# Kernel optimization log

Hardware: AMD Instinct MI355X
Metric: run time of the kernel (lower is better)

## Reference

```python
import jax, jax.numpy as jnp
import numpy as np

H = 1024      # hidden_dim
NH = 16       # num_heads
HD = H // NH  # head_dim
FFN = 4096
EPS = 1e-5


def setup_inputs() -> dict:
    key = jax.random.key(0)
    ks = jax.random.split(key, 12)
    s = 0.02
    return {
        "x": jax.random.normal(ks[0], (2, 2048, H), dtype=jnp.float32),
        "w_qkv": jax.random.normal(ks[1], (H, 3 * H), dtype=jnp.float32) * s,
        "b_qkv": jnp.zeros((3 * H,), dtype=jnp.float32),
        "w_out": jax.random.normal(ks[2], (H, H), dtype=jnp.float32) * s,
        "b_out": jnp.zeros((H,), dtype=jnp.float32),
        "ln1_g": jnp.ones((H,), dtype=jnp.float32),
        "ln1_b": jnp.zeros((H,), dtype=jnp.float32),
        "ln2_g": jnp.ones((H,), dtype=jnp.float32),
        "ln2_b": jnp.zeros((H,), dtype=jnp.float32),
        "w1": jax.random.normal(ks[3], (H, FFN), dtype=jnp.float32) * s,
        "b1": jnp.zeros((FFN,), dtype=jnp.float32),
        "w2": jax.random.normal(ks[4], (FFN, H), dtype=jnp.float32) * s,
        "b2": jnp.zeros((H,), dtype=jnp.float32),
    }


def _layernorm(x, g, b):
    mu = jnp.mean(x, axis=-1, keepdims=True)
    var = jnp.mean(jnp.square(x - mu), axis=-1, keepdims=True)
    return (x - mu) * jax.lax.rsqrt(var + EPS) * g + b


def reference(x, w_qkv, b_qkv, w_out, b_out, ln1_g, ln1_b, ln2_g, ln2_b, w1, b1, w2, b2):
    B, S, _ = x.shape
    # pre-LN attention branch
    h = _layernorm(x, ln1_g, ln1_b)
    qkv = h @ w_qkv + b_qkv                       # (B,S,3H)
    qkv = qkv.reshape(B, S, 3, NH, HD).transpose(2, 0, 3, 1, 4)
    q, k, v = qkv[0], qkv[1], qkv[2]              # (B,NH,S,HD)
    scores = jnp.einsum("bhqd,bhkd->bhqk", q, k) / jnp.sqrt(jnp.float32(HD))
    causal = jnp.triu(jnp.ones((S, S), dtype=bool), k=1)
    scores = jnp.where(causal, -jnp.inf, scores)
    attn = jax.nn.softmax(scores, axis=-1)
    out = jnp.einsum("bhqk,bhkd->bhqd", attn, v)  # (B,NH,S,HD)
    out = out.transpose(0, 2, 1, 3).reshape(B, S, H)
    attn_out = out @ w_out + b_out
    x = x + attn_out
    # FFN branch
    h2 = _layernorm(x, ln2_g, ln2_b)
    ffn = jax.nn.gelu(h2 @ w1 + b1, approximate=False) @ w2 + b2
    return x + ffn
```

## Files before the change

### kernel.cpp

```cpp
#include <hip/hip_runtime.h>
#include <hip/hip_bf16.h>

typedef __bf16 bf16_t;
typedef __bf16 bf16x8 __attribute__((ext_vector_type(8)));
typedef __bf16 bf16x4 __attribute__((ext_vector_type(4)));
typedef __bf16 bf16x2 __attribute__((ext_vector_type(2)));
typedef float  f32x4  __attribute__((ext_vector_type(4)));

#define HDIM 1024
#define SEQ  2048
#define NHEAD 16
#define HEADD 64

__device__ __forceinline__ void gld_lds16(const void* g, void* l) {
  __builtin_amdgcn_global_load_lds(
      (const __attribute__((address_space(1))) unsigned int*)g,
      (__attribute__((address_space(3))) unsigned int*)l, 16, 0, 0);
}

__device__ __forceinline__ float fexp2(float x) {
#if __has_builtin(__builtin_amdgcn_exp2f)
  return __builtin_amdgcn_exp2f(x);
#else
  return exp2f(x);
#endif
}

__global__ __launch_bounds__(256) void ln_kernel(const float* __restrict__ x,
                                                 const float* __restrict__ gam,
                                                 const float* __restrict__ bet,
                                                 bf16_t* __restrict__ out) {
  int row = blockIdx.x;
  int t = threadIdx.x;
  const float4* xr = (const float4*)(x + (size_t)row * HDIM);
  float4 v = xr[t];
  float s = v.x + v.y + v.z + v.w;
  float ss = v.x*v.x + v.y*v.y + v.z*v.z + v.w*v.w;
  #pragma unroll
  for (int o = 32; o > 0; o >>= 1) {
    s  += __shfl_xor(s, o);
    ss += __shfl_xor(ss, o);
  }
  __shared__ float red[8];
  int w = t >> 6;
  if ((t & 63) == 0) { red[w*2] = s; red[w*2+1] = ss; }
  __syncthreads();
  s  = red[0] + red[2] + red[4] + red[6];
  ss = red[1] + red[3] + red[5] + red[7];
  float mu  = s * (1.0f / HDIM);
  float var = ss * (1.0f / HDIM) - mu * mu;
  float rstd = rsqrtf(var + 1e-5f);
  float4 g4 = ((const float4*)gam)[t];
  float4 b4 = ((const float4*)bet)[t];
  bf16x4 o4;
  o4[0] = (bf16_t)((v.x - mu) * rstd * g4.x + b4.x);
  o4[1] = (bf16_t)((v.y - mu) * rstd * g4.y + b4.y);
  o4[2] = (bf16_t)((v.z - mu) * rstd * g4.z + b4.z);
  o4[3] = (bf16_t)((v.w - mu) * rstd * g4.w + b4.w);
  *(bf16x4*)(out + (size_t)row * HDIM + t * 4) = o4;
}

__global__ __launch_bounds__(256)
void prep_kernel(const float* __restrict__ w_qkv, bf16_t* __restrict__ wqkvT,
                 const float* __restrict__ w_out, bf16_t* __restrict__ woutT,
                 const float* __restrict__ w1,    bf16_t* __restrict__ w1T,
                 const float* __restrict__ w2,    bf16_t* __restrict__ w2T,
                 const float* __restrict__ x,     const float* __restrict__ ln1_g,
                 const float* __restrict__ ln1_b, bf16_t* __restrict__ ln1o) {
  __shared__ float tile[64][65];
  int bid = blockIdx.x;
  int t = threadIdx.x;
  if (bid >= 3072) {
    int row = bid - 3072;
    const float4* xr = (const float4*)(x + (size_t)row * HDIM);
    float4 v = xr[t];
    float s = v.x + v.y + v.z + v.w;
    float ss = v.x*v.x + v.y*v.y + v.z*v.z + v.w*v.w;
    #pragma unroll
    for (int o = 32; o > 0; o >>= 1) {
      s  += __shfl_xor(s, o);
      ss += __shfl_xor(ss, o);
    }
    float* red = &tile[0][0];
    int w = t >> 6;
    if ((t & 63) == 0) { red[w*2] = s; red[w*2+1] = ss; }
    __syncthreads();
    s  = red[0] + red[2] + red[4] + red[6];
    ss = red[1] + red[3] + red[5] + red[7];
    float mu  = s * (1.0f / HDIM);
    float var = ss * (1.0f / HDIM) - mu * mu;
    float rstd = rsqrtf(var + 1e-5f);
    float4 g4 = ((const float4*)ln1_g)[t];
    float4 b4 = ((const float4*)ln1_b)[t];
    bf16x4 o4;
    o4[0] = (bf16_t)((v.x - mu) * rstd * g4.x + b4.x);
    o4[1] = (bf16_t)((v.y - mu) * rstd * g4.y + b4.y);
    o4[2] = (bf16_t)((v.z - mu) * rstd * g4.z + b4.z);
    o4[3] = (bf16_t)((v.w - mu) * rstd * g4.w + b4.w);
    *(bf16x4*)(ln1o + (size_t)row * HDIM + t * 4) = o4;
    return;
  }
  const float* W; bf16_t* Wt; int Kd, Nd, nbx;
  if (bid < 768)        { W = w_qkv; Wt = wqkvT; Kd = 1024; Nd = 3072; nbx = 48; }
  else if (bid < 1024)  { bid -= 768;  W = w_out; Wt = woutT; Kd = 1024; Nd = 1024; nbx = 16; }
  else if (bid < 2048)  { bid -= 1024; W = w1;    Wt = w1T;   Kd = 1024; Nd = 4096; nbx = 64; }
  else                  { bid -= 2048; W = w2;    Wt = w2T;   Kd = 4096; Nd = 1024; nbx = 16; }
  int n0 = (bid % nbx) * 64, k0 = (bid / nbx) * 64;

  int tx = t & 15, ty = t >> 4;
  #pragma unroll
  for (int i = 0; i < 4; i++) {
    float4 v = *(const float4*)(W + (size_t)(k0 + ty + i*16) * Nd + n0 + tx*4);
    tile[ty + i*16][tx*4 + 0] = v.x;
    tile[ty + i*16][tx*4 + 1] = v.y;
    tile[ty + i*16][tx*4 + 2] = v.z;
    tile[ty + i*16][tx*4 + 3] = v.w;
  }
  __syncthreads();
  #pragma unroll
  for (int i = 0; i < 4; i++) {
    int r = ty + i*16;
    bf16x4 o4;
    o4[0] = (bf16_t)tile[tx*4 + 0][r];
    o4[1] = (bf16_t)tile[tx*4 + 1][r];
    o4[2] = (bf16_t)tile[tx*4 + 2][r];
    o4[3] = (bf16_t)tile[tx*4 + 3][r];
    *(bf16x4*)(Wt + (size_t)(n0 + r) * Kd + k0 + tx*4) = o4;
  }
}

__device__ __forceinline__ float gelu_fast(float x) {
  float y = 0.7978845608f * (x + 0.044715f * x * x * x);
  float u = fexp2(y * 2.885390082f);
  float th = 1.0f - 2.0f * __builtin_amdgcn_rcpf(u + 1.0f);
  return 0.5f * x * (1.0f + th);
}

__global__ __launch_bounds__(256)
void reduce2_kernel(const bf16_t* __restrict__ p0, const bf16_t* __restrict__ p1,
                    const float* __restrict__ bias, const float* __restrict__ resid,
                    float* __restrict__ out) {
  size_t base = ((size_t)blockIdx.x * 256 + threadIdx.x) * 8;
  bf16x8 a = *(const bf16x8*)(p0 + base);
  bf16x8 b = *(const bf16x8*)(p1 + base);
  int col = (int)(base & (HDIM - 1));
  float4 bi0 = *(const float4*)(bias + col);
  float4 bi1 = *(const float4*)(bias + col + 4);
  float4 r0 = *(const float4*)(resid + base);
  float4 r1 = *(const float4*)(resid + base + 4);
  float4 o0, o1;
  o0.x = (float)a[0] + (float)b[0] + bi0.x + r0.x;
  o0.y = (float)a[1] + (float)b[1] + bi0.y + r0.y;
  o0.z = (float)a[2] + (float)b[2] + bi0.z + r0.z;
  o0.w = (float)a[3] + (float)b[3] + bi0.w + r0.w;
  o1.x = (float)a[4] + (float)b[4] + bi1.x + r1.x;
  o1.y = (float)a[5] + (float)b[5] + bi1.y + r1.y;
  o1.z = (float)a[6] + (float)b[6] + bi1.z + r1.z;
  o1.w = (float)a[7] + (float)b[7] + bi1.w + r1.w;
  *(float4*)(out + base)     = o0;
  *(float4*)(out + base + 4) = o1;
}

template<int EPI, int BN, int BK, int WPEU, int SPLITK>
__global__ __launch_bounds__(256, WPEU)
void gemm_bt(const bf16_t* __restrict__ A, const bf16_t* __restrict__ Bt,
             const float* __restrict__ bias, const float* __restrict__ resid,
             void* __restrict__ outp, int M, int N, int K) {
  constexpr int NFRAG = BN / 32;
  constexpr int CH  = BK / 8;
  constexpr int SWZ = CH - 1;
  constexpr int RSH = (BK == 32) ? 1 : 0;
  constexpr int RPP = 256 / CH;
  __shared__ bf16_t As[2][128*BK];
  __shared__ bf16_t Bs[2][BN*BK];
  int t = threadIdx.x;
  int w = t >> 6, l = t & 63;
  int wr = w >> 1, wc = w & 1;

  int nbx = gridDim.x;
  int bid = blockIdx.y * nbx + blockIdx.x;
  int chunkx = (nbx * gridDim.y) >> 3;
  int nb = (bid & 7) * chunkx + (bid >> 3);
  int bm = nb / nbx, bn = nb % nbx;
  size_t m0 = (size_t)bm * 128, n0 = (size_t)bn * BN;

  const int KK = (SPLITK > 1) ? K / SPLITK : K;
  const size_t koff = (SPLITK > 1) ? (size_t)blockIdx.z * KK : 0;

  f32x4 acc[4][NFRAG];
  #pragma unroll
  for (int m = 0; m < 4; m++)
    #pragma unroll
    for (int n = 0; n < NFRAG; n++) acc[m][n] = (f32x4)(0.0f);

  int srow = t / CH;
  int scol = ((t & SWZ) ^ ((srow >> RSH) & SWZ)) * 8;
  int dsto = t * 8;
  const bf16_t* ag = A  + (m0 + srow) * K + koff + scol;
  const bf16_t* bg = Bt + (n0 + srow) * K + koff + scol;

  int lr = l & 15, lg = l >> 4;

  auto stage = [&](int buf, int k0) {
    #pragma unroll
    for (int p = 0; p < 128/RPP; p++)
      gld_lds16(ag + k0 + (size_t)(p*RPP)*K, &As[buf][dsto + p*RPP*BK]);
    #pragma unroll
    for (int p = 0; p < BN/RPP; p++)
      gld_lds16(bg + k0 + (size_t)(p*RPP)*K, &Bs[buf][dsto + p*RPP*BK]);
  };

  stage(0, 0);
  __syncthreads();
  int cur = 0;
  const int NK = KK / BK;
  for (int k = 0; k < NK; k++) {
    if (k + 1 < NK) stage(cur ^ 1, (k + 1) * BK);
    #pragma unroll
    for (int kk = 0; kk < BK/32; kk++) {
      bf16x8 af[4], bfr[NFRAG];
      #pragma unroll
      for (int m = 0; m < 4; m++) {
        int row = wr*64 + m*16 + lr;
        int off = row*BK*2 + (((kk*4 + lg) ^ ((row >> RSH) & SWZ)) << 4);
        af[m] = *(const bf16x8*)((const char*)&As[cur][0] + off);
      }
      #pragma unroll
      for (int n = 0; n < NFRAG; n++) {
        int row = wc*(BN/2) + n*16 + lr;
        int off = row*BK*2 + (((kk*4 + lg) ^ ((row >> RSH) & SWZ)) << 4);
        bfr[n] = *(const bf16x8*)((const char*)&Bs[cur][0] + off);
      }
      #pragma unroll
      for (int m = 0; m < 4; m++)
        #pragma unroll
        for (int n = 0; n < NFRAG; n++)
          acc[m][n] = __builtin_amdgcn_mfma_f32_16x16x32_bf16(af[m], bfr[n], acc[m][n], 0, 0, 0);
    }
    __syncthreads();
    cur ^= 1;
  }

  int r0 = (l >> 4) * 4, c0 = l & 15;
  bf16_t* pd = nullptr;
  if (EPI == 3)
    pd = (bf16_t*)(blockIdx.z == 0 ? outp : (void*)resid);
  #pragma unroll
  for (int m = 0; m < 4; m++) {
    #pragma unroll
    for (int n = 0; n < NFRAG; n++) {
      size_t row = m0 + wr*64 + m*16 + r0;
      size_t col = n0 + wc*(BN/2) + n*16 + c0;
      float bv = (EPI == 3) ? 0.0f : bias[col];
      #pragma unroll
      for (int r = 0; r < 4; r++) {
        float vv = acc[m][n][r] + bv;
        size_t idx = (row + r) * (size_t)N + col;
        if (EPI == 0) {
          ((bf16_t*)outp)[idx] = (bf16_t)vv;
        } else if (EPI == 1) {
          ((float*)outp)[idx] = vv + resid[idx];
        } else if (EPI == 2) {
          ((bf16_t*)outp)[idx] = (bf16_t)gelu_fast(vv);
        } else {
          pd[idx] = (bf16_t)vv;
        }
      }
    }
  }
}

__global__ __launch_bounds__(512, 4)
void attn_kernel(const bf16_t* __restrict__ qkv, bf16_t* __restrict__ out) {
  int idx = blockIdx.x;
  int half = idx >> 8;
  int sub = idx & 255;
  int qth = sub >> 5;
  int qt = half ? qth : (15 - qth);
  int bh = sub & 31;
  int b = bh >> 4, h = bh & 15;
  int t = threadIdx.x, w = t >> 6, l = t & 63;

  __shared__ bf16_t Ks[2][64*64];
  __shared__ bf16_t Vt[2][64*72];
  __shared__ bf16_t Ps[8][16*64];

  const size_t RS = 3 * HDIM;
  const bf16_t* qb = qkv + (size_t)b * SEQ * RS + h * HEADD;
  const bf16_t* kb = qb + HDIM;
  const bf16_t* vb = qb + 2 * HDIM;

  int lr = l & 15, lg = l >> 4;
  const float SCALE = 0.125f * 1.44269504f;

  bf16x8 qf[2];
  {
    size_t qrow = (size_t)qt * 128 + w * 16 + lr;
    qf[0] = *(const bf16x8*)(qb + qrow * RS + lg * 8);
    qf[1] = *(const bf16x8*)(qb + qrow * RS + 32 + lg * 8);
    #pragma unroll
    for (int i = 0; i < 8; i++) {
      qf[0][i] = (bf16_t)((float)qf[0][i] * SCALE);
      qf[1][i] = (bf16_t)((float)qf[1][i] * SCALE);
    }
  }

  f32x4 o[4];
  #pragma unroll
  for (int d = 0; d < 4; d++) o[d] = (f32x4)(0.0f);
  float m = -1e30f, lsum = 0.0f;

  int srow = t >> 3, scol = (t & 7) * 8;
  int Fv = ((scol >> 3) & 7) << 3;
  int nkt = 2 * qt + 2;

  const bf16_t* kg0 = kb + (size_t)srow * RS + scol;
  const bf16_t* vg0 = vb + (size_t)srow * RS + scol;

  bf16x8 kr = *(const bf16x8*)kg0;
  bf16x8 vr = *(const bf16x8*)vg0;

  int wrow0 = qt * 128 + w * 16;
  int qg = wrow0 + lr;
  bf16_t* pw = Ps[w];
  int psw = (lr & 7) << 4;
  int cur = 0;

  for (int kt = 0; kt < nkt; kt++) {
    {
      int ba = srow * 128 + scol * 2;
      int sw = (srow & 7) << 4;
      *(bf16x8*)((char*)Ks[cur] + (ba ^ sw)) = kr;
      int ksw = srow ^ Fv;
      bf16_t* vt = Vt[cur];
      #pragma unroll
      for (int i = 0; i < 8; i++)
        vt[(scol + i) * 72 + ksw] = vr[i];
    }
    if (kt + 1 < nkt) {
      kr = *(const bf16x8*)(kg0 + (size_t)(kt + 1) * 64 * RS);
      vr = *(const bf16x8*)(vg0 + (size_t)(kt + 1) * 64 * RS);
    }
    asm volatile("s_waitcnt lgkmcnt(0)" ::: "memory");
    __builtin_amdgcn_s_barrier();
    __builtin_amdgcn_sched_barrier(0);

    bool skipw = (kt * 64) > (wrow0 + 15);
    if (!skipw) {
      f32x4 sc[4];
      __builtin_amdgcn_s_setprio(1);
      #pragma unroll
      for (int kt2 = 0; kt2 < 4; kt2++) {
        sc[kt2] = (f32x4)(0.0f);
        #pragma unroll
        for (int kk = 0; kk < 2; kk++) {
          int row = kt2 * 16 + lr;
          int off = (row * 128 + kk * 64 + lg * 16) ^ ((row & 7) << 4);
          bf16x8 kf = *(const bf16x8*)((char*)Ks[cur] + off);
          sc[kt2] = __builtin_amdgcn_mfma_f32_16x16x32_bf16(kf, qf[kk], sc[kt2], 0, 0, 0);
        }
      }
      __builtin_amdgcn_s_setprio(0);
      if (kt * 64 + 63 > wrow0) {
        #pragma unroll
        for (int kt2 = 0; kt2 < 4; kt2++) {
          #pragma unroll
          for (int r = 0; r < 4; r++) {
            int kcol = kt*64 + kt2*16 + lg*4 + r;
            if (kcol > qg) sc[kt2][r] = -1e30f;
          }
        }
      }
      float tm0 = fmaxf(fmaxf(sc[0][0], sc[0][1]), fmaxf(sc[0][2], sc[0][3]));
      float tm1 = fmaxf(fmaxf(sc[1][0], sc[1][1]), fmaxf(sc[1][2], sc[1][3]));
      float tm2 = fmaxf(fmaxf(sc[2][0], sc[2][1]), fmaxf(sc[2][2], sc[2][3]));
      float tm3 = fmaxf(fmaxf(sc[3][0], sc[3][1]), fmaxf(sc[3][2], sc[3][3]));
      float tm = fmaxf(fmaxf(tm0, tm1), fmaxf(tm2, tm3));
      tm = fmaxf(tm, __shfl_xor(tm, 16));
      tm = fmaxf(tm, __shfl_xor(tm, 32));
      if (!__all(tm <= m + 8.0f)) {
        float nm = fmaxf(m, tm);
        float alpha = fexp2(m - nm);
        m = nm;
        lsum *= alpha;
        #pragma unroll
        for (int d = 0; d < 4; d++)
          #pragma unroll
          for (int r = 0; r < 4; r++) o[d][r] *= alpha;
      }
      #pragma unroll
      for (int kt2 = 0; kt2 < 4; kt2++) {
        float p0 = fexp2(sc[kt2][0] - m);
        float p1 = fexp2(sc[kt2][1] - m);
        float p2 = fexp2(sc[kt2][2] - m);
        float p3 = fexp2(sc[kt2][3] - m);
        lsum += (p0 + p1) + (p2 + p3);
        bf16x2 pa; pa[0] = (bf16_t)p0; pa[1] = (bf16_t)p1;
        bf16x2 pb; pb[0] = (bf16_t)p2; pb[1] = (bf16_t)p3;
        int base = lr * 128 + kt2 * 32 + lg * 8;
        *(bf16x2*)((char*)pw + ((base)     ^ psw)) = pa;
        *(bf16x2*)((char*)pw + ((base + 4) ^ psw)) = pb;
      }
      asm volatile("s_waitcnt lgkmcnt(0)" ::: "memory");
      __builtin_amdgcn_s_setprio(1);
      #pragma unroll
      for (int kk = 0; kk < 2; kk++) {
        int poff = (lr * 128 + kk * 64 + lg * 16) ^ psw;
        bf16x8 pf = *(const bf16x8*)((char*)pw + poff);
        #pragma unroll
        for (int dblk = 0; dblk < 4; dblk++) {
          int vrow = dblk * 16 + lr;
          int Fd = ((vrow >> 3) & 7) << 3;
          bf16x8 vf = *(const bf16x8*)(Vt[cur] + vrow * 72 + ((kk * 32 + lg * 8) ^ Fd));
          o[dblk] = __builtin_amdgcn_mfma_f32_16x16x32_bf16(vf, pf, o[dblk], 0, 0, 0);
        }
      }
      __builtin_amdgcn_s_setprio(0);
    }
    cur ^= 1;
  }

  lsum += __shfl_xor(lsum, 16);
  lsum += __shfl_xor(lsum, 32);
  float inv = 1.0f / lsum;

  bf16_t* ob = out + ((size_t)b * SEQ + qg) * HDIM + h * HEADD;
  #pragma unroll
  for (int dblk = 0; dblk < 4; dblk++) {
    bf16x4 q4;
    #pragma unroll
    for (int r = 0; r < 4; r++) q4[r] = (bf16_t)(o[dblk][r] * inv);
    *(bf16x4*)(ob + dblk * 16 + lg * 4) = q4;
  }
}

extern "C" void kernel_launch(void* const* d_in, const int* in_sizes, int n_in,
                              void* d_out, int out_size, void* d_ws, size_t ws_size,
                              hipStream_t stream) {
  (void)in_sizes; (void)n_in; (void)out_size; (void)ws_size;
  const float* x     = (const float*)d_in[0];
  const float* w_qkv = (const float*)d_in[1];
  const float* b_qkv = (const float*)d_in[2];
  const float* w_out = (const float*)d_in[3];
  const float* b_out = (const float*)d_in[4];
  const float* ln1_g = (const float*)d_in[5];
  const float* ln1_b = (const float*)d_in[6];
  const float* ln2_g = (const float*)d_in[7];
  const float* ln2_b = (const float*)d_in[8];
  const float* w1    = (const float*)d_in[9];
  const float* b1    = (const float*)d_in[10];
  const float* w2    = (const float*)d_in[11];
  const float* b2    = (const float*)d_in[12];
  float* out = (float*)d_out;

  char* ws = (char*)d_ws;
  size_t off = 0;
  auto alloc = [&](size_t bytes) -> void* {
    void* p = ws + off;
    off += (bytes + 255) & ~(size_t)255;
    return p;
  };
  bf16_t* wqkvT = (bf16_t*)alloc((size_t)3072*1024*2);
  bf16_t* woutT = (bf16_t*)alloc((size_t)1024*1024*2);
  bf16_t* w1T   = (bf16_t*)alloc((size_t)4096*1024*2);
  bf16_t* w2T   = (bf16_t*)alloc((size_t)1024*4096*2);
  bf16_t* ln1o  = (bf16_t*)alloc((size_t)4096*1024*2);
  bf16_t* qkvb  = (bf16_t*)alloc((size_t)4096*4096*2);
  bf16_t* attno = (bf16_t*)alloc((size_t)4096*1024*2);
  float*  x2    = (float*) alloc((size_t)4096*1024*4);
  bf16_t* h2 = ln1o;
  bf16_t* g  = qkvb;
  bf16_t* part0 = ln1o;
  bf16_t* part1 = attno;

  dim3 blk(256);
  prep_kernel<<<7168, blk, 0, stream>>>(w_qkv, wqkvT, w_out, woutT, w1, w1T, w2, w2T,
                                        x, ln1_g, ln1_b, ln1o);
  gemm_bt<0,128,32,4,1><<<dim3(24, 32), blk, 0, stream>>>(ln1o, wqkvT, b_qkv, nullptr, qkvb, 4096, 3072, 1024);
  attn_kernel<<<512, dim3(512), 0, stream>>>(qkvb, attno);
  gemm_bt<1,64,64,2,1><<<dim3(16, 32), blk, 0, stream>>>(attno, woutT, b_out, x, x2, 4096, 1024, 1024);
  ln_kernel<<<4096, blk, 0, stream>>>(x2, ln2_g, ln2_b, h2);
  gemm_bt<2,128,32,4,1><<<dim3(32, 32), blk, 0, stream>>>(h2, w1T, b1, nullptr, g, 4096, 4096, 1024);
  gemm_bt<3,128,64,2,2><<<dim3(8, 32, 2), blk, 0, stream>>>(g, w2T, b2, (const float*)part1, part0, 4096, 1024, 4096);
  reduce2_kernel<<<2048, blk, 0, stream>>>(part0, part1, b2, x2, out);
}
```

Before: 209.2 us.

## Pair complementary causal query tiles per attention block to share K/V loads

Each attention block now handles two query tiles, a high one (15-pr) and a low one (pr), and streams the K/V tiles once for both. The low tile reuses the first K/V tiles loaded for the high tile, which halves K/V global traffic and gives every block the same amount of causal work. The grid drops from 512 to 256 blocks and the launch-bounds occupancy hint goes from 4 to 2, since each thread now holds two sets of Q fragments and accumulators. The risks are fewer resident waves to hide latency and only 256 blocks to spread across the CUs.

```diff
diff --git a/kernel.cpp b/kernel.cpp
--- a/kernel.cpp
+++ b/kernel.cpp
@@ -270,14 +270,12 @@
   }
 }
 
-__global__ __launch_bounds__(512, 4)
+__global__ __launch_bounds__(512, 2)
 void attn_kernel(const bf16_t* __restrict__ qkv, bf16_t* __restrict__ out) {
-  int idx = blockIdx.x;
-  int half = idx >> 8;
-  int sub = idx & 255;
-  int qth = sub >> 5;
-  int qt = half ? qth : (15 - qth);
-  int bh = sub & 31;
+  int bid = blockIdx.x;
+  int pr = bid >> 5;
+  int bh = bid & 31;
+  int Qhi = 15 - pr, Qlo = pr;
   int b = bh >> 4, h = bh & 15;
   int t = threadIdx.x, w = t >> 6, l = t & 63;
 
@@ -293,26 +291,32 @@
   int lr = l & 15, lg = l >> 4;
   const float SCALE = 0.125f * 1.44269504f;
 
-  bf16x8 qf[2];
+  bf16x8 qfh[2], qfl[2];
   {
-    size_t qrow = (size_t)qt * 128 + w * 16 + lr;
-    qf[0] = *(const bf16x8*)(qb + qrow * RS + lg * 8);
-    qf[1] = *(const bf16x8*)(qb + qrow * RS + 32 + lg * 8);
+    size_t qrh = (size_t)Qhi * 128 + w * 16 + lr;
+    size_t qrl = (size_t)Qlo * 128 + w * 16 + lr;
+    qfh[0] = *(const bf16x8*)(qb + qrh * RS + lg * 8);
+    qfh[1] = *(const bf16x8*)(qb + qrh * RS + 32 + lg * 8);
+    qfl[0] = *(const bf16x8*)(qb + qrl * RS + lg * 8);
+    qfl[1] = *(const bf16x8*)(qb + qrl * RS + 32 + lg * 8);
     #pragma unroll
     for (int i = 0; i < 8; i++) {
-      qf[0][i] = (bf16_t)((float)qf[0][i] * SCALE);
-      qf[1][i] = (bf16_t)((float)qf[1][i] * SCALE);
-    }
-  }
-
-  f32x4 o[4];
-  #pragma unroll
-  for (int d = 0; d < 4; d++) o[d] = (f32x4)(0.0f);
-  float m = -1e30f, lsum = 0.0f;
+      qfh[0][i] = (bf16_t)((float)qfh[0][i] * SCALE);
+      qfh[1][i] = (bf16_t)((float)qfh[1][i] * SCALE);
+      qfl[0][i] = (bf16_t)((float)qfl[0][i] * SCALE);
+      qfl[1][i] = (bf16_t)((float)qfl[1][i] * SCALE);
+    }
+  }
+
+  f32x4 oh[4], ol[4];
+  #pragma unroll
+  for (int d = 0; d < 4; d++) { oh[d] = (f32x4)(0.0f); ol[d] = (f32x4)(0.0f); }
+  float mh = -1e30f, lsh = 0.0f, ml = -1e30f, lsl = 0.0f;
 
   int srow = t >> 3, scol = (t & 7) * 8;
   int Fv = ((scol >> 3) & 7) << 3;
-  int nkt = 2 * qt + 2;
+  int nkt = 2 * Qhi + 2;
+  int nkt_lo = 2 * Qlo + 2;
 
   const bf16_t* kg0 = kb + (size_t)srow * RS + scol;
   const bf16_t* vg0 = vb + (size_t)srow * RS + scol;
@@ -320,11 +324,86 @@
   bf16x8 kr = *(const bf16x8*)kg0;
   bf16x8 vr = *(const bf16x8*)vg0;
 
-  int wrow0 = qt * 128 + w * 16;
-  int qg = wrow0 + lr;
+  int wrow_h = Qhi * 128 + w * 16;
+  int wrow_l = Qlo * 128 + w * 16;
+  int qgh = wrow_h + lr;
+  int qgl = wrow_l + lr;
   bf16_t* pw = Ps[w];
   int psw = (lr & 7) << 4;
   int cur = 0;
+
+  auto softpv = [&](int kt, const bf16x8 (&qf)[2], f32x4 (&o)[4],
+                    float& m, float& lsum, int wrow0, int qg) {
+    f32x4 sc[4];
+    __builtin_amdgcn_s_setprio(1);
+    #pragma unroll
+    for (int kt2 = 0; kt2 < 4; kt2++) {
+      sc[kt2] = (f32x4)(0.0f);
+      #pragma unroll
+      for (int kk = 0; kk < 2; kk++) {
+        int row = kt2 * 16 + lr;
+        int off = (row * 128 + kk * 64 + lg * 16) ^ ((row & 7) << 4);
+        bf16x8 kf = *(const bf16x8*)((char*)Ks[cur] + off);
+        sc[kt2] = __builtin_amdgcn_mfma_f32_16x16x32_bf16(kf, qf[kk], sc[kt2], 0, 0, 0);
+      }
+    }
+    __builtin_amdgcn_s_setprio(0);
+    if (kt * 64 + 63 > wrow0) {
+      #pragma unroll
+      for (int kt2 = 0; kt2 < 4; kt2++) {
+        #pragma unroll
+        for (int r = 0; r < 4; r++) {
+          int kcol = kt*64 + kt2*16 + lg*4 + r;
+          if (kcol > qg) sc[kt2][r] = -1e30f;
+        }
+      }
+    }
+    float tm0 = fmaxf(fmaxf(sc[0][0], sc[0][1]), fmaxf(sc[0][2], sc[0][3]));
+    float tm1 = fmaxf(fmaxf(sc[1][0], sc[1][1]), fmaxf(sc[1][2], sc[1][3]));
+    float tm2 = fmaxf(fmaxf(sc[2][0], sc[2][1]), fmaxf(sc[2][2], sc[2][3]));
+    float tm3 = fmaxf(fmaxf(sc[3][0], sc[3][1]), fmaxf(sc[3][2], sc[3][3]));
+    float tm = fmaxf(fmaxf(tm0, tm1), fmaxf(tm2, tm3));
+    tm = fmaxf(tm, __shfl_xor(tm, 16));
+    tm = fmaxf(tm, __shfl_xor(tm, 32));
+    if (!__all(tm <= m + 8.0f)) {
+      float nm = fmaxf(m, tm);
+      float alpha = fexp2(m - nm);
+      m = nm;
+      lsum *= alpha;
+      #pragma unroll
+      for (int d = 0; d < 4; d++)
+        #pragma unroll
+        for (int r = 0; r < 4; r++) o[d][r] *= alpha;
+    }
+    #pragma unroll
+    for (int kt2 = 0; kt2 < 4; kt2++) {
+      float p0 = fexp2(sc[kt2][0] - m);
+      float p1 = fexp2(sc[kt2][1] - m);
+      float p2 = fexp2(sc[kt2][2] - m);
+      float p3 = fexp2(sc[kt2][3] - m);
+      lsum += (p0 + p1) + (p2 + p3);
+      bf16x2 pa; pa[0] = (bf16_t)p0; pa[1] = (bf16_t)p1;
+      bf16x2 pb; pb[0] = (bf16_t)p2; pb[1] = (bf16_t)p3;
+      int base = lr * 128 + kt2 * 32 + lg * 8;
+      *(bf16x2*)((char*)pw + ((base)     ^ psw)) = pa;
+      *(bf16x2*)((char*)pw + ((base + 4) ^ psw)) = pb;
+    }
+    asm volatile("s_waitcnt lgkmcnt(0)" ::: "memory");
+    __builtin_amdgcn_s_setprio(1);
+    #pragma unroll
+    for (int kk = 0; kk < 2; kk++) {
+      int poff = (lr * 128 + kk * 64 + lg * 16) ^ psw;
+      bf16x8 pf = *(const bf16x8*)((char*)pw + poff);
+      #pragma unroll
+      for (int dblk = 0; dblk < 4; dblk++) {
+        int vrow = dblk * 16 + lr;
+        int Fd = ((vrow >> 3) & 7) << 3;
+        bf16x8 vf = *(const bf16x8*)(Vt[cur] + vrow * 72 + ((kk * 32 + lg * 8) ^ Fd));
+        o[dblk] = __builtin_amdgcn_mfma_f32_16x16x32_bf16(vf, pf, o[dblk], 0, 0, 0);
+      }
+    }
+    __builtin_amdgcn_s_setprio(0);
+  };
 
   for (int kt = 0; kt < nkt; kt++) {
     {
@@ -345,92 +424,33 @@
     __builtin_amdgcn_s_barrier();
     __builtin_amdgcn_sched_barrier(0);
 
-    bool skipw = (kt * 64) > (wrow0 + 15);
-    if (!skipw) {
-      f32x4 sc[4];
-      __builtin_amdgcn_s_setprio(1);
-      #pragma unroll
-      for (int kt2 = 0; kt2 < 4; kt2++) {
-        sc[kt2] = (f32x4)(0.0f);
-        #pragma unroll
-        for (int kk = 0; kk < 2; kk++) {
-          int row = kt2 * 16 + lr;
-          int off = (row * 128 + kk * 64 + lg * 16) ^ ((row & 7) << 4);
-          bf16x8 kf = *(const bf16x8*)((char*)Ks[cur] + off);
-          sc[kt2] = __builtin_amdgcn_mfma_f32_16x16x32_bf16(kf, qf[kk], sc[kt2], 0, 0, 0);
-        }
-      }
-      __builtin_amdgcn_s_setprio(0);
-      if (kt * 64 + 63 > wrow0) {
-        #pragma unroll
-        for (int kt2 = 0; kt2 < 4; kt2++) {
-          #pragma unroll
-          for (int r = 0; r < 4; r++) {
-            int kcol = kt*64 + kt2*16 + lg*4 + r;
-            if (kcol > qg) sc[kt2][r] = -1e30f;
-          }
-        }
-      }
-      float tm0 = fmaxf(fmaxf(sc[0][0], sc[0][1]), fmaxf(sc[0][2], sc[0][3]));
-      float tm1 = fmaxf(fmaxf(sc[1][0], sc[1][1]), fmaxf(sc[1][2], sc[1][3]));
-      float tm2 = fmaxf(fmaxf(sc[2][0], sc[2][1]), fmaxf(sc[2][2], sc[2][3]));
-      float tm3 = fmaxf(fmaxf(sc[3][0], sc[3][1]), fmaxf(sc[3][2], sc[3][3]));
-      float tm = fmaxf(fmaxf(tm0, tm1), fmaxf(tm2, tm3));
-      tm = fmaxf(tm, __shfl_xor(tm, 16));
-      tm = fmaxf(tm, __shfl_xor(tm, 32));
-      if (!__all(tm <= m + 8.0f)) {
-        float nm = fmaxf(m, tm);
-        float alpha = fexp2(m - nm);
-        m = nm;
-        lsum *= alpha;
-        #pragma unroll
-        for (int d = 0; d < 4; d++)
-          #pragma unroll
-          for (int r = 0; r < 4; r++) o[d][r] *= alpha;
-      }
-      #pragma unroll
-      for (int kt2 = 0; kt2 < 4; kt2++) {
-        float p0 = fexp2(sc[kt2][0] - m);
-        float p1 = fexp2(sc[kt2][1] - m);
-        float p2 = fexp2(sc[kt2][2] - m);
-        float p3 = fexp2(sc[kt2][3] - m);
-        lsum += (p0 + p1) + (p2 + p3);
-        bf16x2 pa; pa[0] = (bf16_t)p0; pa[1] = (bf16_t)p1;
-        bf16x2 pb; pb[0] = (bf16_t)p2; pb[1] = (bf16_t)p3;
-        int base = lr * 128 + kt2 * 32 + lg * 8;
-        *(bf16x2*)((char*)pw + ((base)     ^ psw)) = pa;
-        *(bf16x2*)((char*)pw + ((base + 4) ^ psw)) = pb;
-      }
-      asm volatile("s_waitcnt lgkmcnt(0)" ::: "memory");
-      __builtin_amdgcn_s_setprio(1);
-      #pragma unroll
-      for (int kk = 0; kk < 2; kk++) {
-        int poff = (lr * 128 + kk * 64 + lg * 16) ^ psw;
-        bf16x8 pf = *(const bf16x8*)((char*)pw + poff);
-        #pragma unroll
-        for (int dblk = 0; dblk < 4; dblk++) {
-          int vrow = dblk * 16 + lr;
-          int Fd = ((vrow >> 3) & 7) << 3;
-          bf16x8 vf = *(const bf16x8*)(Vt[cur] + vrow * 72 + ((kk * 32 + lg * 8) ^ Fd));
-          o[dblk] = __builtin_amdgcn_mfma_f32_16x16x32_bf16(vf, pf, o[dblk], 0, 0, 0);
-        }
-      }
-      __builtin_amdgcn_s_setprio(0);
-    }
+    if (!((kt * 64) > (wrow_h + 15)))
+      softpv(kt, qfh, oh, mh, lsh, wrow_h, qgh);
+    if (kt < nkt_lo && !((kt * 64) > (wrow_l + 15)))
+      softpv(kt, qfl, ol, ml, lsl, wrow_l, qgl);
+
     cur ^= 1;
   }
 
-  lsum += __shfl_xor(lsum, 16);
-  lsum += __shfl_xor(lsum, 32);
-  float inv = 1.0f / lsum;
-
-  bf16_t* ob = out + ((size_t)b * SEQ + qg) * HDIM + h * HEADD;
+  lsh += __shfl_xor(lsh, 16);
+  lsh += __shfl_xor(lsh, 32);
+  lsl += __shfl_xor(lsl, 16);
+  lsl += __shfl_xor(lsl, 32);
+  float invh = 1.0f / lsh;
+  float invl = 1.0f / lsl;
+
+  bf16_t* obh = out + ((size_t)b * SEQ + qgh) * HDIM + h * HEADD;
+  bf16_t* obl = out + ((size_t)b * SEQ + qgl) * HDIM + h * HEADD;
   #pragma unroll
   for (int dblk = 0; dblk < 4; dblk++) {
-    bf16x4 q4;
-    #pragma unroll
-    for (int r = 0; r < 4; r++) q4[r] = (bf16_t)(o[dblk][r] * inv);
-    *(bf16x4*)(ob + dblk * 16 + lg * 4) = q4;
+    bf16x4 qh4, ql4;
+    #pragma unroll
+    for (int r = 0; r < 4; r++) {
+      qh4[r] = (bf16_t)(oh[dblk][r] * invh);
+      ql4[r] = (bf16_t)(ol[dblk][r] * invl);
+    }
+    *(bf16x4*)(obh + dblk * 16 + lg * 4) = qh4;
+    *(bf16x4*)(obl + dblk * 16 + lg * 4) = ql4;
   }
 }
 
@@ -477,7 +497,7 @@
   prep_kernel<<<7168, blk, 0, stream>>>(w_qkv, wqkvT, w_out, woutT, w1, w1T, w2, w2T,
                                         x, ln1_g, ln1_b, ln1o);
   gemm_bt<0,128,32,4,1><<<dim3(24, 32), blk, 0, stream>>>(ln1o, wqkvT, b_qkv, nullptr, qkvb, 4096, 3072, 1024);
-  attn_kernel<<<512, dim3(512), 0, stream>>>(qkvb, attno);
+  attn_kernel<<<256, dim3(512), 0, stream>>>(qkvb, attno);
   gemm_bt<1,64,64,2,1><<<dim3(16, 32), blk, 0, stream>>>(attno, woutT, b_out, x, x2, 4096, 1024, 1024);
   ln_kernel<<<4096, blk, 0, stream>>>(x2, ln2_g, ln2_b, h2);
   gemm_bt<2,128,32,4,1><<<dim3(32, 32), blk, 0, stream>>>(h2, w1T, b1, nullptr, g, 4096, 4096, 1024);
```

New measurement: 213.7 us. 1.02x slower.
